# Kernel tuning notes

Measured on AMD Instinct MI355X. Metric: run time of the kernel, lower is better.

The kernel has to match this reference:

```python
import jax, jax.numpy as jnp
import numpy as np

N = 20000      # nodes
E = 640000     # edges
IN = 2         # in_dim
H = 4          # heads
C = 64         # hidden_dim (per-head channels)
ED = 3         # edge_dim
K = 4          # num_clusters
EPS = 1e-16    # PyG softmax eps


def setup_inputs():
    key = jax.random.key(0)
    ks = jax.random.split(key, 32)
    g = lambda i, sh: (jax.random.normal(ks[i], sh, dtype=jnp.float32) * 0.1)
    inp = {
        'x': jax.random.normal(ks[0], (N, IN), dtype=jnp.float32),
        'edge_index': jax.random.randint(ks[1], (2, E), 0, N, dtype=jnp.int64),
        'edge_attr': jax.random.normal(ks[2], (E, ED), dtype=jnp.float32),
        # input_proj
        'Wp': g(3, (IN, C)), 'bp': g(4, (C,)),
        # conv1: in C -> H*C, concat
        'W1': g(5, (C, H * C)), 'We1': g(6, (ED, H * C)),
        'as1': g(7, (H, C)), 'ad1': g(8, (H, C)), 'ae1': g(9, (H, C)), 'b1': g(10, (H * C,)),
        # conv2: in H*C -> H*C, concat
        'W2': g(11, (H * C, H * C)), 'We2': g(12, (ED, H * C)),
        'as2': g(13, (H, C)), 'ad2': g(14, (H, C)), 'ae2': g(15, (H, C)), 'b2': g(16, (H * C,)),
        # conv3: in H*C -> C, heads=1
        'W3': g(17, (H * C, C)), 'We3': g(18, (ED, C)),
        'as3': g(19, (1, C)), 'ad3': g(20, (1, C)), 'ae3': g(21, (1, C)), 'b3': g(22, (C,)),
        # classifier
        'Wc': g(23, (C, K)), 'bc': g(24, (K,)),
    }
    return inp


def _gat(h, src, dst, edge_attr, W, We, a_src, a_dst, a_edge, bias, heads, cph):
    """PyG GATConv (shared lin for src/dst, edge_dim, concat=True), eval mode."""
    xh = (h @ W).reshape(N, heads, cph)                       # [N,H,C]
    alpha_src = jnp.einsum('nhc,hc->nh', xh, a_src)           # [N,H]
    alpha_dst = jnp.einsum('nhc,hc->nh', xh, a_dst)
    eh = (edge_attr @ We).reshape(E, heads, cph)              # [E,H,C]
    alpha = alpha_src[src] + alpha_dst[dst] + jnp.einsum('ehc,hc->eh', eh, a_edge)
    alpha = jax.nn.leaky_relu(alpha, 0.2)                     # [E,H]
    # segment softmax over destination neighborhoods
    m = jax.ops.segment_max(alpha, dst, num_segments=N)       # [N,H]
    ea = jnp.exp(alpha - m[dst])
    s = jax.ops.segment_sum(ea, dst, num_segments=N)
    attn = ea / (s[dst] + EPS)                                # [E,H]
    msg = xh[src] * attn[:, :, None]                          # [E,H,C]
    out = jax.ops.segment_sum(msg, dst, num_segments=N)       # [N,H,C]
    return out.reshape(N, heads * cph) + bias


def reference(x, edge_index, edge_attr, Wp, bp,
              W1, We1, as1, ad1, ae1, b1,
              W2, We2, as2, ad2, ae2, b2,
              W3, We3, as3, ad3, ae3, b3,
              Wc, bc):
    src, dst = edge_index[0], edge_index[1]
    h = jax.nn.elu(x @ Wp + bp)
    h = jax.nn.elu(_gat(h, src, dst, edge_attr, W1, We1, as1, ad1, ae1, b1, H, C))
    h = jax.nn.elu(_gat(h, src, dst, edge_attr, W2, We2, as2, ad2, ae2, b2, H, C))
    h = _gat(h, src, dst, edge_attr, W3, We3, as3, ad3, ae3, b3, 1, C)
    return jax.nn.softmax(h @ Wc + bc, axis=-1)
```

## Files before the change

### kernel.cpp

```cpp
#include <hip/hip_runtime.h>
#include <math.h>

#define N_NODES 20000
#define N_EDGES 640000

typedef __attribute__((ext_vector_type(8))) short short8;
typedef __attribute__((ext_vector_type(4))) float floatx4;
typedef __attribute__((ext_vector_type(2))) float float2v;

__device__ __forceinline__ float elu_f(float v) { return v > 0.f ? v : expm1f(v); }

__device__ __forceinline__ unsigned short bf16_rne(float f) {
  union { float f; unsigned u; } v;
  v.f = f;
  unsigned r = v.u + 0x7FFF + ((v.u >> 16) & 1);
  return (unsigned short)(r >> 16);
}

__device__ __forceinline__ float2v unpack_bf2(unsigned u) {
  union { unsigned u; float f; } lo, hi;
  lo.u = u << 16;
  hi.u = u & 0xffff0000u;
  return (float2v){lo.f, hi.f};
}

__device__ __forceinline__ int swz(int c) {
  return (c & ~7) | ((((c & 7) + ((c >> 3) >> 2))) & 7);
}


__global__ void hist_kernel(const int* __restrict__ dst, int* __restrict__ cnt, int ne) {
  int e = blockIdx.x * 256 + threadIdx.x;
  if (e < ne) atomicAdd(&cnt[dst[e]], 1);
}

__global__ __launch_bounds__(1024) void scan_kernel(const int* __restrict__ cnt,
                                                    int* __restrict__ row_ptr,
                                                    int* __restrict__ row_next, int n) {
  __shared__ int part[1024];
  int t = threadIdx.x;
  int per = (n + 1023) / 1024;
  int base = t * per;
  int v[20];
  if (base + per <= n) {
    #pragma unroll
    for (int q = 0; q < 5; ++q) {
      int4 u = *(const int4*)(cnt + base + q * 4);
      v[q * 4 + 0] = u.x; v[q * 4 + 1] = u.y; v[q * 4 + 2] = u.z; v[q * 4 + 3] = u.w;
    }
  } else {
    #pragma unroll
    for (int i = 0; i < 20; ++i) v[i] = (base + i < n) ? cnt[base + i] : 0;
  }
  int local = 0;
  #pragma unroll
  for (int i = 0; i < 20; ++i) local += v[i];
  part[t] = local;
  __syncthreads();
  for (int off = 1; off < 1024; off <<= 1) {
    int pv = (t >= off) ? part[t - off] : 0;
    __syncthreads();
    part[t] += pv;
    __syncthreads();
  }
  int prefix = (t == 0) ? 0 : part[t - 1];
  #pragma unroll
  for (int i = 0; i < 20; ++i) {
    int idx = base + i;
    if (idx < n) {
      row_ptr[idx] = prefix;
      row_next[idx] = prefix;
      prefix += v[i];
    }
  }
  if (t == 1023) row_ptr[n] = part[1023];
}

__global__ void fill_kernel(const int* __restrict__ dst, int* __restrict__ row_next,
                            int* __restrict__ csr_eid, int ne) {
  int e = blockIdx.x * 256 + threadIdx.x;
  if (e >= ne) return;
  int pos = atomicAdd(&row_next[dst[e]], 1);
  csr_eid[pos] = e;
}


__global__ void prep_all_kernel(const float* __restrict__ x, const float* __restrict__ Wp,
                                const float* __restrict__ bp, unsigned short* __restrict__ h_bf,
                                const float* __restrict__ W1, const float* __restrict__ W2,
                                const float* __restrict__ W3, unsigned short* __restrict__ Bt1,
                                unsigned short* __restrict__ Bt2, unsigned short* __restrict__ Bt3,
                                const float* __restrict__ We1, const float* __restrict__ ae1,
                                const float* __restrict__ We2, const float* __restrict__ ae2,
                                const float* __restrict__ We3, const float* __restrict__ ae3,
                                const int* __restrict__ csr_eid, const int* __restrict__ src,
                                const float* __restrict__ ea, int* __restrict__ csr_src,
                                float* __restrict__ edot) {
  int b = blockIdx.x, t = threadIdx.x;
  if (b < 5000) {
    int i = b * 256 + t;
    int node = i >> 6, c = i & 63;
    float v = x[node * 2] * Wp[c] + x[node * 2 + 1] * Wp[64 + c] + bp[c];
    h_bf[i] = bf16_rne(elu_f(v));
  } else if (b < 5384) {
    int idx = (b - 5000) * 256 + t;
    const float* W; unsigned short* Bt; int K, Nc, local;
    if (idx < 16384)      { W = W1; Bt = Bt1; K = 64;  Nc = 256; local = idx; }
    else if (idx < 81920) { W = W2; Bt = Bt2; K = 256; Nc = 256; local = idx - 16384; }
    else if (idx < 98304) { W = W3; Bt = Bt3; K = 256; Nc = 64;  local = idx - 81920; }
    else return;
    int k = local / Nc, n = local - k * Nc;
    Bt[(size_t)n * K + k] = bf16_rne(W[local]);
  } else {
    __shared__ float pj[27];
    if (t < 12) {
      int d = t >> 2, h = t & 3;
      float s = 0.f;
      for (int c = 0; c < 64; ++c) s += We1[d * 256 + h * 64 + c] * ae1[h * 64 + c];
      pj[t] = s;
    } else if (t < 24) {
      int u = t - 12; int d = u >> 2, h = u & 3;
      float s = 0.f;
      for (int c = 0; c < 64; ++c) s += We2[d * 256 + h * 64 + c] * ae2[h * 64 + c];
      pj[12 + u] = s;
    } else if (t < 27) {
      int d = t - 24;
      float s = 0.f;
      for (int c = 0; c < 64; ++c) s += We3[d * 64 + c] * ae3[c];
      pj[24 + d] = s;
    }
    __syncthreads();
    int i = (b - 5384) * 256 + t;
    if (i >= N_EDGES) return;
    int eid = csr_eid[i];
    csr_src[i] = src[eid];
    float e0 = ea[eid * 3 + 0], e1 = ea[eid * 3 + 1], e2 = ea[eid * 3 + 2];
    #pragma unroll
    for (int h = 0; h < 4; ++h)
      edot[(size_t)h * N_EDGES + i] = e0 * pj[h] + e1 * pj[4 + h] + e2 * pj[8 + h];
    #pragma unroll
    for (int h = 0; h < 4; ++h)
      edot[(size_t)(4 + h) * N_EDGES + i] = e0 * pj[12 + h] + e1 * pj[16 + h] + e2 * pj[20 + h];
    edot[(size_t)8 * N_EDGES + i] = e0 * pj[24] + e1 * pj[25] + e2 * pj[26];
  }
}


template <int KDIM>
__global__ __launch_bounds__(256) void mfma_gemm_alpha_kernel(
    const unsigned short* __restrict__ A, const unsigned short* __restrict__ Bt,
    unsigned short* __restrict__ C_bf, const float* __restrict__ a_src,
    const float* __restrict__ a_dst, float* __restrict__ alp_s,
    float* __restrict__ alp_d, int M, int Nc) {
  __shared__ unsigned short As[64][40];
  __shared__ unsigned short Bs[64][40];
  int t = threadIdx.x;
  int wave = t >> 6, lane = t & 63;
  int m_frag = lane & 15, quad = lane >> 4;
  int row0 = blockIdx.y * 64, col0 = blockIdx.x * 64;
  int lr = t >> 2;
  int lk = (t & 3) * 8;
  floatx4 acc[4];
  #pragma unroll
  for (int c = 0; c < 4; ++c) acc[c] = (floatx4){0.f, 0.f, 0.f, 0.f};

  for (int k0 = 0; k0 < KDIM; k0 += 32) {
    int gr = row0 + lr;
    short8 av = {0, 0, 0, 0, 0, 0, 0, 0};
    if (gr < M) av = *(const short8*)(A + (size_t)gr * KDIM + k0 + lk);
    *(short8*)(&As[lr][lk]) = av;
    short8 bv = *(const short8*)(Bt + (size_t)(col0 + lr) * KDIM + k0 + lk);
    *(short8*)(&Bs[lr][lk]) = bv;
    __syncthreads();
    short8 a = *(const short8*)(&As[wave * 16 + m_frag][quad * 8]);
    #pragma unroll
    for (int c = 0; c < 4; ++c) {
      short8 b = *(const short8*)(&Bs[c * 16 + m_frag][quad * 8]);
      acc[c] = __builtin_amdgcn_mfma_f32_16x16x32_bf16(a, b, acc[c], 0, 0, 0);
    }
    __syncthreads();
  }

  int H = Nc >> 6;
  int head = blockIdx.x;
  float ps[4] = {}, pd[4] = {};
  #pragma unroll
  for (int c = 0; c < 4; ++c) {
    float asv = a_src[head * 64 + c * 16 + m_frag];
    float adv = a_dst[head * 64 + c * 16 + m_frag];
    #pragma unroll
    for (int i = 0; i < 4; ++i) {
      ps[i] += acc[c][i] * asv;
      pd[i] += acc[c][i] * adv;
    }
  }
  #pragma unroll
  for (int off = 1; off < 16; off <<= 1) {
    #pragma unroll
    for (int i = 0; i < 4; ++i) {
      ps[i] += __shfl_xor(ps[i], off);
      pd[i] += __shfl_xor(pd[i], off);
    }
  }
  #pragma unroll
  for (int c = 0; c < 4; ++c) {
    #pragma unroll
    for (int i = 0; i < 4; ++i) {
      int gr = row0 + wave * 16 + quad * 4 + i;
      if (gr < M) C_bf[(size_t)gr * Nc + col0 + c * 16 + m_frag] = bf16_rne(acc[c][i]);
    }
  }
  if (m_frag == 0) {
    #pragma unroll
    for (int i = 0; i < 4; ++i) {
      int gr = row0 + wave * 16 + quad * 4 + i;
      if (gr < M) {
        alp_s[gr * H + head] = ps[i];
        alp_d[gr * H + head] = pd[i];
      }
    }
  }
}


template <bool OUT_BF>
__global__ __launch_bounds__(256) void softagg4_kernel(
    const int* __restrict__ row_ptr, const int* __restrict__ csr_src,
    const float* __restrict__ edot, const float* __restrict__ alp_s,
    const float* __restrict__ alp_d, const unsigned short* __restrict__ xh_bf,
    const float* __restrict__ bias, float* __restrict__ out,
    unsigned short* __restrict__ out_bf) {
  constexpr int HC = 256, H = 4, CHUNK = 256, L = 32, S = 8;
  __shared__ float lds_w[H][CHUNK + 8];
  __shared__ int lds_src[CHUNK];
  __shared__ float sh_inv[H];
  __shared__ float red[4 * HC];

  int n = blockIdx.x;
  int t = threadIdx.x;
  int wave = t >> 6, lane = t & 63;
  int slot = t / L, l = t % L;
  int head2 = l >> 3;
  int s0 = row_ptr[n], s1 = row_ptr[n + 1];

  float s_run = 0.f;
  float2v accp[4] = {};
  float adv = alp_d[n * H + wave];
  const float* __restrict__ edot_h = edot + (size_t)wave * N_EDGES;

  for (int c0 = s0; c0 < s1; c0 += CHUNK) {
    int cend = min(s1, c0 + CHUNK);
    {
      float se = 0.f;
      for (int i = c0 + lane; i < cend; i += 64) {
        int s = csr_src[i];
        if (wave == 0) lds_src[i - c0] = s;
        float a = alp_s[s * H + wave] + adv + edot_h[i];
        a = a > 0.f ? a : 0.2f * a;
        float w = __expf(fminf(a, 30.f));
        lds_w[wave][i - c0] = w;
        se += w;
      }
      #pragma unroll
      for (int off = 1; off < 64; off <<= 1) se += __shfl_xor(se, off);
      s_run += se;
    }
    __syncthreads();
    int i = c0 + slot;
    for (; i + S < cend; i += 2 * S) {
      int sA = lds_src[i - c0];
      int sB = lds_src[i - c0 + S];
      float wA = lds_w[head2][i - c0];
      float wB = lds_w[head2][i - c0 + S];
      uint4 uA = *(const uint4*)(xh_bf + (size_t)sA * HC + l * 8);
      uint4 uB = *(const uint4*)(xh_bf + (size_t)sB * HC + l * 8);
      float2v wAp = {wA, wA}, wBp = {wB, wB};
      accp[0] = __builtin_elementwise_fma(unpack_bf2(uA.x), wAp, accp[0]);
      accp[1] = __builtin_elementwise_fma(unpack_bf2(uA.y), wAp, accp[1]);
      accp[2] = __builtin_elementwise_fma(unpack_bf2(uA.z), wAp, accp[2]);
      accp[3] = __builtin_elementwise_fma(unpack_bf2(uA.w), wAp, accp[3]);
      accp[0] = __builtin_elementwise_fma(unpack_bf2(uB.x), wBp, accp[0]);
      accp[1] = __builtin_elementwise_fma(unpack_bf2(uB.y), wBp, accp[1]);
      accp[2] = __builtin_elementwise_fma(unpack_bf2(uB.z), wBp, accp[2]);
      accp[3] = __builtin_elementwise_fma(unpack_bf2(uB.w), wBp, accp[3]);
    }
    if (i < cend) {
      int s = lds_src[i - c0];
      float w = lds_w[head2][i - c0];
      uint4 u = *(const uint4*)(xh_bf + (size_t)s * HC + l * 8);
      float2v wp = {w, w};
      accp[0] = __builtin_elementwise_fma(unpack_bf2(u.x), wp, accp[0]);
      accp[1] = __builtin_elementwise_fma(unpack_bf2(u.y), wp, accp[1]);
      accp[2] = __builtin_elementwise_fma(unpack_bf2(u.z), wp, accp[2]);
      accp[3] = __builtin_elementwise_fma(unpack_bf2(u.w), wp, accp[3]);
    }
    __syncthreads();
  }
  if (lane == 0) sh_inv[wave] = 1.0f / (s_run + 1e-16f);
  __syncthreads();
  float2v invp = {sh_inv[head2], sh_inv[head2]};
  #pragma unroll
  for (int d = 0; d < 4; ++d) accp[d] *= invp;
  float accf[8];
  #pragma unroll
  for (int d = 0; d < 4; ++d) { accf[2 * d] = accp[d].x; accf[2 * d + 1] = accp[d].y; }
  #pragma unroll
  for (int off = L; off < 64; off <<= 1) {
    #pragma unroll
    for (int j = 0; j < 8; ++j) accf[j] += __shfl_xor(accf[j], off);
  }
  if (lane < L) {
    #pragma unroll
    for (int j = 0; j < 8; ++j) red[wave * HC + swz(lane * 8 + j)] = accf[j];
  }
  __syncthreads();
  {
    int pos = swz(t);
    float a = red[0 * HC + pos] + red[1 * HC + pos] + red[2 * HC + pos] + red[3 * HC + pos];
    a += bias[t];
    a = elu_f(a);
    if (OUT_BF) out_bf[(size_t)n * HC + t] = bf16_rne(a);
    else out[(size_t)n * HC + t] = a;
  }
}


__global__ __launch_bounds__(256) void softagg_cls_kernel(
    const int* __restrict__ row_ptr, const int* __restrict__ csr_src,
    const float* __restrict__ edot, const float* __restrict__ alp_s,
    const float* __restrict__ alp_d, const unsigned short* __restrict__ xh_bf,
    const float* __restrict__ b3, const float* __restrict__ Wc,
    const float* __restrict__ bc, float* __restrict__ out, int n_nodes) {
  constexpr int CHUNK = 256;
  __shared__ float lds_w[4][CHUNK];
  __shared__ int lds_s[4][CHUNK];

  int wave = threadIdx.x >> 6, lane = threadIdx.x & 63;
  int n = blockIdx.x * 4 + wave;
  if (n >= n_nodes) return;
  int slot = lane >> 3, l = lane & 7;
  int s0 = row_ptr[n], s1 = row_ptr[n + 1];

  float s_run = 0.f;
  float2v accp[4] = {};
  float adv = alp_d[n];

  for (int c0 = s0; c0 < s1; c0 += CHUNK) {
    int cend = min(s1, c0 + CHUNK);
    float se = 0.f;
    for (int i = c0 + lane; i < cend; i += 64) {
      int s = csr_src[i];
      lds_s[wave][i - c0] = s;
      float a = alp_s[s] + adv + edot[i];
      a = a > 0.f ? a : 0.2f * a;
      float w = __expf(fminf(a, 30.f));
      lds_w[wave][i - c0] = w;
      se += w;
    }
    #pragma unroll
    for (int off = 1; off < 64; off <<= 1) se += __shfl_xor(se, off);
    s_run += se;
    int i = c0 + slot;
    for (; i + 8 < cend; i += 16) {
      int sA = lds_s[wave][i - c0];
      int sB = lds_s[wave][i - c0 + 8];
      float wA = lds_w[wave][i - c0];
      float wB = lds_w[wave][i - c0 + 8];
      uint4 uA = *(const uint4*)(xh_bf + (size_t)sA * 64 + l * 8);
      uint4 uB = *(const uint4*)(xh_bf + (size_t)sB * 64 + l * 8);
      float2v wAp = {wA, wA}, wBp = {wB, wB};
      accp[0] = __builtin_elementwise_fma(unpack_bf2(uA.x), wAp, accp[0]);
      accp[1] = __builtin_elementwise_fma(unpack_bf2(uA.y), wAp, accp[1]);
      accp[2] = __builtin_elementwise_fma(unpack_bf2(uA.z), wAp, accp[2]);
      accp[3] = __builtin_elementwise_fma(unpack_bf2(uA.w), wAp, accp[3]);
      accp[0] = __builtin_elementwise_fma(unpack_bf2(uB.x), wBp, accp[0]);
      accp[1] = __builtin_elementwise_fma(unpack_bf2(uB.y), wBp, accp[1]);
      accp[2] = __builtin_elementwise_fma(unpack_bf2(uB.z), wBp, accp[2]);
      accp[3] = __builtin_elementwise_fma(unpack_bf2(uB.w), wBp, accp[3]);
    }
    if (i < cend) {
      int s = lds_s[wave][i - c0];
      float w = lds_w[wave][i - c0];
      uint4 u = *(const uint4*)(xh_bf + (size_t)s * 64 + l * 8);
      float2v wp = {w, w};
      accp[0] = __builtin_elementwise_fma(unpack_bf2(u.x), wp, accp[0]);
      accp[1] = __builtin_elementwise_fma(unpack_bf2(u.y), wp, accp[1]);
      accp[2] = __builtin_elementwise_fma(unpack_bf2(u.z), wp, accp[2]);
      accp[3] = __builtin_elementwise_fma(unpack_bf2(u.w), wp, accp[3]);
    }
  }
  float inv = 1.0f / (s_run + 1e-16f);
  float2v invp = {inv, inv};
  #pragma unroll
  for (int d = 0; d < 4; ++d) accp[d] *= invp;
  float accf[8];
  #pragma unroll
  for (int d = 0; d < 4; ++d) { accf[2 * d] = accp[d].x; accf[2 * d + 1] = accp[d].y; }
  #pragma unroll
  for (int off = 8; off < 64; off <<= 1) {
    #pragma unroll
    for (int j = 0; j < 8; ++j) accf[j] += __shfl_xor(accf[j], off);
  }
  float p0 = 0.f, p1 = 0.f, p2 = 0.f, p3 = 0.f;
  #pragma unroll
  for (int j = 0; j < 8; ++j) {
    int c = l * 8 + j;
    float v = accf[j] + b3[c];
    p0 += v * Wc[c * 4 + 0];
    p1 += v * Wc[c * 4 + 1];
    p2 += v * Wc[c * 4 + 2];
    p3 += v * Wc[c * 4 + 3];
  }
  #pragma unroll
  for (int off = 1; off < 8; off <<= 1) {
    p0 += __shfl_xor(p0, off);
    p1 += __shfl_xor(p1, off);
    p2 += __shfl_xor(p2, off);
    p3 += __shfl_xor(p3, off);
  }
  if (lane == 0) {
    p0 += bc[0]; p1 += bc[1]; p2 += bc[2]; p3 += bc[3];
    float mx = fmaxf(fmaxf(p0, p1), fmaxf(p2, p3));
    float e0 = __expf(p0 - mx), e1 = __expf(p1 - mx), e2 = __expf(p2 - mx), e3 = __expf(p3 - mx);
    float s = 1.f / (e0 + e1 + e2 + e3);
    out[n * 4 + 0] = e0 * s;
    out[n * 4 + 1] = e1 * s;
    out[n * 4 + 2] = e2 * s;
    out[n * 4 + 3] = e3 * s;
  }
}


extern "C" void kernel_launch(void* const* d_in, const int* in_sizes, int n_in,
                              void* d_out, int out_size, void* d_ws, size_t ws_size,
                              hipStream_t stream) {
  const float* x   = (const float*)d_in[0];
  const int*   ei  = (const int*)d_in[1];
  const float* ea  = (const float*)d_in[2];
  const float* Wp  = (const float*)d_in[3];
  const float* bp  = (const float*)d_in[4];
  const float* W1  = (const float*)d_in[5];
  const float* We1 = (const float*)d_in[6];
  const float* as1 = (const float*)d_in[7];
  const float* ad1 = (const float*)d_in[8];
  const float* ae1 = (const float*)d_in[9];
  const float* b1  = (const float*)d_in[10];
  const float* W2  = (const float*)d_in[11];
  const float* We2 = (const float*)d_in[12];
  const float* as2 = (const float*)d_in[13];
  const float* ad2 = (const float*)d_in[14];
  const float* ae2 = (const float*)d_in[15];
  const float* b2  = (const float*)d_in[16];
  const float* W3  = (const float*)d_in[17];
  const float* We3 = (const float*)d_in[18];
  const float* as3 = (const float*)d_in[19];
  const float* ad3 = (const float*)d_in[20];
  const float* ae3 = (const float*)d_in[21];
  const float* b3  = (const float*)d_in[22];
  const float* Wc  = (const float*)d_in[23];
  const float* bc  = (const float*)d_in[24];
  float* out = (float*)d_out;

  const int* src = ei;
  const int* dst = ei + N_EDGES;

  char* wptr = (char*)d_ws;
  auto alloc = [&](size_t bytes) {
    char* p = wptr;
    wptr += (bytes + 255) & ~(size_t)255;
    return p;
  };
  int*            cnt      = (int*)alloc((size_t)N_NODES * 4);
  int*            row_ptr  = (int*)alloc((size_t)(N_NODES + 1) * 4);
  int*            row_next = (int*)alloc((size_t)N_NODES * 4);
  int*            csr_eid  = (int*)alloc((size_t)N_EDGES * 4);
  int*            csr_src  = (int*)alloc((size_t)N_EDGES * 4);
  float*          edot     = (float*)alloc((size_t)9 * N_EDGES * 4);
  unsigned short* hA_bf    = (unsigned short*)alloc((size_t)N_NODES * 256 * 2);
  unsigned short* hX_bf    = (unsigned short*)alloc((size_t)N_NODES * 256 * 2);
  float*          alp_s    = (float*)alloc((size_t)N_NODES * 4 * 4);
  float*          alp_d    = (float*)alloc((size_t)N_NODES * 4 * 4);
  unsigned short* Bt1      = (unsigned short*)alloc((size_t)64 * 256 * 2);
  unsigned short* Bt2      = (unsigned short*)alloc((size_t)256 * 256 * 2);
  unsigned short* Bt3      = (unsigned short*)alloc((size_t)256 * 64 * 2);

  hipMemsetAsync(cnt, 0, (size_t)N_NODES * 4, stream);
  hist_kernel<<<(N_EDGES + 255) / 256, 256, 0, stream>>>(dst, cnt, N_EDGES);
  scan_kernel<<<1, 1024, 0, stream>>>(cnt, row_ptr, row_next, N_NODES);
  fill_kernel<<<(N_EDGES + 255) / 256, 256, 0, stream>>>(dst, row_next, csr_eid, N_EDGES);

  prep_all_kernel<<<5384 + (N_EDGES + 255) / 256, 256, 0, stream>>>(
      x, Wp, bp, hA_bf, W1, W2, W3, Bt1, Bt2, Bt3,
      We1, ae1, We2, ae2, We3, ae3, csr_eid, src, ea, csr_src, edot);

  dim3 g256(4, (N_NODES + 63) / 64);
  dim3 g64(1, (N_NODES + 63) / 64);

  mfma_gemm_alpha_kernel<64><<<g256, 256, 0, stream>>>(hA_bf, Bt1, hX_bf, as1, ad1,
                                                       alp_s, alp_d, N_NODES, 256);
  softagg4_kernel<true><<<N_NODES, 256, 0, stream>>>(row_ptr, csr_src,
                                                     edot + (size_t)0 * N_EDGES,
                                                     alp_s, alp_d, hX_bf, b1, nullptr, hA_bf);

  mfma_gemm_alpha_kernel<256><<<g256, 256, 0, stream>>>(hA_bf, Bt2, hX_bf, as2, ad2,
                                                        alp_s, alp_d, N_NODES, 256);
  softagg4_kernel<true><<<N_NODES, 256, 0, stream>>>(row_ptr, csr_src,
                                                     edot + (size_t)4 * N_EDGES,
                                                     alp_s, alp_d, hX_bf, b2, nullptr, hA_bf);

  mfma_gemm_alpha_kernel<256><<<g64, 256, 0, stream>>>(hA_bf, Bt3, hX_bf, as3, ad3,
                                                       alp_s, alp_d, N_NODES, 64);
  softagg_cls_kernel<<<(N_NODES + 3) / 4, 256, 0, stream>>>(row_ptr, csr_src,
                                                            edot + (size_t)8 * N_EDGES,
                                                            alp_s, alp_d, hX_bf, b3, Wc, bc,
                                                            out, N_NODES);
}
```

Measured before the change: 377.5 us.

## Store edge attention terms in bf16, enlarge GEMM row tile, raise occupancy hints

Edge-attention dot products are stored as bf16 instead of fp32, which halves the traffic for the 9xE edot array that is written in prep and read by every aggregation kernel. The MFMA GEMM now computes 128 rows per block, two 16-row fragments per wave, so each B tile is reused twice and the grid is halved. The aggregation kernels also get launch_bounds with a minimum of 8 blocks per CU to push the compiler toward fewer registers and higher occupancy. The risks are reduced precision in the attention logits and possible register spills from the occupancy hint.

```diff
diff --git a/kernel.cpp b/kernel.cpp
--- a/kernel.cpp
+++ b/kernel.cpp
@@ -15,6 +15,12 @@
   v.f = f;
   unsigned r = v.u + 0x7FFF + ((v.u >> 16) & 1);
   return (unsigned short)(r >> 16);
+}
+
+__device__ __forceinline__ float bf_to_f(unsigned short u) {
+  union { unsigned u; float f; } v;
+  v.u = (unsigned)u << 16;
+  return v.f;
 }
 
 __device__ __forceinline__ float2v unpack_bf2(unsigned u) {
@@ -95,7 +101,7 @@
                                 const float* __restrict__ We3, const float* __restrict__ ae3,
                                 const int* __restrict__ csr_eid, const int* __restrict__ src,
                                 const float* __restrict__ ea, int* __restrict__ csr_src,
-                                float* __restrict__ edot) {
+                                unsigned short* __restrict__ edot) {
   int b = blockIdx.x, t = threadIdx.x;
   if (b < 5000) {
     int i = b * 256 + t;
@@ -137,11 +143,12 @@
     float e0 = ea[eid * 3 + 0], e1 = ea[eid * 3 + 1], e2 = ea[eid * 3 + 2];
     #pragma unroll
     for (int h = 0; h < 4; ++h)
-      edot[(size_t)h * N_EDGES + i] = e0 * pj[h] + e1 * pj[4 + h] + e2 * pj[8 + h];
+      edot[(size_t)h * N_EDGES + i] = bf16_rne(e0 * pj[h] + e1 * pj[4 + h] + e2 * pj[8 + h]);
     #pragma unroll
     for (int h = 0; h < 4; ++h)
-      edot[(size_t)(4 + h) * N_EDGES + i] = e0 * pj[12 + h] + e1 * pj[16 + h] + e2 * pj[20 + h];
-    edot[(size_t)8 * N_EDGES + i] = e0 * pj[24] + e1 * pj[25] + e2 * pj[26];
+      edot[(size_t)(4 + h) * N_EDGES + i] =
+          bf16_rne(e0 * pj[12 + h] + e1 * pj[16 + h] + e2 * pj[20 + h]);
+    edot[(size_t)8 * N_EDGES + i] = bf16_rne(e0 * pj[24] + e1 * pj[25] + e2 * pj[26]);
   }
 }
 
@@ -152,81 +159,91 @@
     unsigned short* __restrict__ C_bf, const float* __restrict__ a_src,
     const float* __restrict__ a_dst, float* __restrict__ alp_s,
     float* __restrict__ alp_d, int M, int Nc) {
-  __shared__ unsigned short As[64][40];
+  __shared__ unsigned short As[128][40];
   __shared__ unsigned short Bs[64][40];
   int t = threadIdx.x;
   int wave = t >> 6, lane = t & 63;
   int m_frag = lane & 15, quad = lane >> 4;
-  int row0 = blockIdx.y * 64, col0 = blockIdx.x * 64;
+  int row0 = blockIdx.y * 128, col0 = blockIdx.x * 64;
   int lr = t >> 2;
   int lk = (t & 3) * 8;
-  floatx4 acc[4];
-  #pragma unroll
-  for (int c = 0; c < 4; ++c) acc[c] = (floatx4){0.f, 0.f, 0.f, 0.f};
+  floatx4 acc[2][4];
+  #pragma unroll
+  for (int g = 0; g < 2; ++g)
+    #pragma unroll
+    for (int c = 0; c < 4; ++c) acc[g][c] = (floatx4){0.f, 0.f, 0.f, 0.f};
 
   for (int k0 = 0; k0 < KDIM; k0 += 32) {
-    int gr = row0 + lr;
-    short8 av = {0, 0, 0, 0, 0, 0, 0, 0};
-    if (gr < M) av = *(const short8*)(A + (size_t)gr * KDIM + k0 + lk);
-    *(short8*)(&As[lr][lk]) = av;
+    #pragma unroll
+    for (int g = 0; g < 2; ++g) {
+      int gr = row0 + g * 64 + lr;
+      short8 av = {0, 0, 0, 0, 0, 0, 0, 0};
+      if (gr < M) av = *(const short8*)(A + (size_t)gr * KDIM + k0 + lk);
+      *(short8*)(&As[g * 64 + lr][lk]) = av;
+    }
     short8 bv = *(const short8*)(Bt + (size_t)(col0 + lr) * KDIM + k0 + lk);
     *(short8*)(&Bs[lr][lk]) = bv;
     __syncthreads();
-    short8 a = *(const short8*)(&As[wave * 16 + m_frag][quad * 8]);
+    short8 a0 = *(const short8*)(&As[wave * 32 + m_frag][quad * 8]);
+    short8 a1 = *(const short8*)(&As[wave * 32 + 16 + m_frag][quad * 8]);
     #pragma unroll
     for (int c = 0; c < 4; ++c) {
       short8 b = *(const short8*)(&Bs[c * 16 + m_frag][quad * 8]);
-      acc[c] = __builtin_amdgcn_mfma_f32_16x16x32_bf16(a, b, acc[c], 0, 0, 0);
+      acc[0][c] = __builtin_amdgcn_mfma_f32_16x16x32_bf16(a0, b, acc[0][c], 0, 0, 0);
+      acc[1][c] = __builtin_amdgcn_mfma_f32_16x16x32_bf16(a1, b, acc[1][c], 0, 0, 0);
     }
     __syncthreads();
   }
 
   int H = Nc >> 6;
   int head = blockIdx.x;
-  float ps[4] = {}, pd[4] = {};
-  #pragma unroll
-  for (int c = 0; c < 4; ++c) {
-    float asv = a_src[head * 64 + c * 16 + m_frag];
-    float adv = a_dst[head * 64 + c * 16 + m_frag];
-    #pragma unroll
-    for (int i = 0; i < 4; ++i) {
-      ps[i] += acc[c][i] * asv;
-      pd[i] += acc[c][i] * adv;
-    }
-  }
-  #pragma unroll
-  for (int off = 1; off < 16; off <<= 1) {
-    #pragma unroll
-    for (int i = 0; i < 4; ++i) {
-      ps[i] += __shfl_xor(ps[i], off);
-      pd[i] += __shfl_xor(pd[i], off);
-    }
-  }
-  #pragma unroll
-  for (int c = 0; c < 4; ++c) {
-    #pragma unroll
-    for (int i = 0; i < 4; ++i) {
-      int gr = row0 + wave * 16 + quad * 4 + i;
-      if (gr < M) C_bf[(size_t)gr * Nc + col0 + c * 16 + m_frag] = bf16_rne(acc[c][i]);
-    }
-  }
-  if (m_frag == 0) {
-    #pragma unroll
-    for (int i = 0; i < 4; ++i) {
-      int gr = row0 + wave * 16 + quad * 4 + i;
-      if (gr < M) {
-        alp_s[gr * H + head] = ps[i];
-        alp_d[gr * H + head] = pd[i];
+  #pragma unroll
+  for (int g = 0; g < 2; ++g) {
+    float ps[4] = {}, pd[4] = {};
+    #pragma unroll
+    for (int c = 0; c < 4; ++c) {
+      float asv = a_src[head * 64 + c * 16 + m_frag];
+      float adv = a_dst[head * 64 + c * 16 + m_frag];
+      #pragma unroll
+      for (int i = 0; i < 4; ++i) {
+        ps[i] += acc[g][c][i] * asv;
+        pd[i] += acc[g][c][i] * adv;
       }
     }
+    #pragma unroll
+    for (int off = 1; off < 16; off <<= 1) {
+      #pragma unroll
+      for (int i = 0; i < 4; ++i) {
+        ps[i] += __shfl_xor(ps[i], off);
+        pd[i] += __shfl_xor(pd[i], off);
+      }
+    }
+    #pragma unroll
+    for (int c = 0; c < 4; ++c) {
+      #pragma unroll
+      for (int i = 0; i < 4; ++i) {
+        int gr = row0 + wave * 32 + g * 16 + quad * 4 + i;
+        if (gr < M) C_bf[(size_t)gr * Nc + col0 + c * 16 + m_frag] = bf16_rne(acc[g][c][i]);
+      }
+    }
+    if (m_frag == 0) {
+      #pragma unroll
+      for (int i = 0; i < 4; ++i) {
+        int gr = row0 + wave * 32 + g * 16 + quad * 4 + i;
+        if (gr < M) {
+          alp_s[gr * H + head] = ps[i];
+          alp_d[gr * H + head] = pd[i];
+        }
+      }
+    }
   }
 }
 
 
 template <bool OUT_BF>
-__global__ __launch_bounds__(256) void softagg4_kernel(
+__global__ __launch_bounds__(256, 8) void softagg4_kernel(
     const int* __restrict__ row_ptr, const int* __restrict__ csr_src,
-    const float* __restrict__ edot, const float* __restrict__ alp_s,
+    const unsigned short* __restrict__ edot, const float* __restrict__ alp_s,
     const float* __restrict__ alp_d, const unsigned short* __restrict__ xh_bf,
     const float* __restrict__ bias, float* __restrict__ out,
     unsigned short* __restrict__ out_bf) {
@@ -246,7 +263,7 @@
   float s_run = 0.f;
   float2v accp[4] = {};
   float adv = alp_d[n * H + wave];
-  const float* __restrict__ edot_h = edot + (size_t)wave * N_EDGES;
+  const unsigned short* __restrict__ edot_h = edot + (size_t)wave * N_EDGES;
 
   for (int c0 = s0; c0 < s1; c0 += CHUNK) {
     int cend = min(s1, c0 + CHUNK);
@@ -255,7 +272,7 @@
       for (int i = c0 + lane; i < cend; i += 64) {
         int s = csr_src[i];
         if (wave == 0) lds_src[i - c0] = s;
-        float a = alp_s[s * H + wave] + adv + edot_h[i];
+        float a = alp_s[s * H + wave] + adv + bf_to_f(edot_h[i]);
         a = a > 0.f ? a : 0.2f * a;
         float w = __expf(fminf(a, 30.f));
         lds_w[wave][i - c0] = w;
@@ -325,9 +342,9 @@
 }
 
 
-__global__ __launch_bounds__(256) void softagg_cls_kernel(
+__global__ __launch_bounds__(256, 8) void softagg_cls_kernel(
     const int* __restrict__ row_ptr, const int* __restrict__ csr_src,
-    const float* __restrict__ edot, const float* __restrict__ alp_s,
+    const unsigned short* __restrict__ edot, const float* __restrict__ alp_s,
     const float* __restrict__ alp_d, const unsigned short* __restrict__ xh_bf,
     const float* __restrict__ b3, const float* __restrict__ Wc,
     const float* __restrict__ bc, float* __restrict__ out, int n_nodes) {
@@ -351,7 +368,7 @@
     for (int i = c0 + lane; i < cend; i += 64) {
       int s = csr_src[i];
       lds_s[wave][i - c0] = s;
-      float a = alp_s[s] + adv + edot[i];
+      float a = alp_s[s] + adv + bf_to_f(edot[i]);
       a = a > 0.f ? a : 0.2f * a;
       float w = __expf(fminf(a, 30.f));
       lds_w[wave][i - c0] = w;
@@ -475,7 +492,7 @@
   int*            row_next = (int*)alloc((size_t)N_NODES * 4);
   int*            csr_eid  = (int*)alloc((size_t)N_EDGES * 4);
   int*            csr_src  = (int*)alloc((size_t)N_EDGES * 4);
-  float*          edot     = (float*)alloc((size_t)9 * N_EDGES * 4);
+  unsigned short* edot     = (unsigned short*)alloc((size_t)9 * N_EDGES * 2);
   unsigned short* hA_bf    = (unsigned short*)alloc((size_t)N_NODES * 256 * 2);
   unsigned short* hX_bf    = (unsigned short*)alloc((size_t)N_NODES * 256 * 2);
   float*          alp_s    = (float*)alloc((size_t)N_NODES * 4 * 4);
@@ -493,8 +510,8 @@
       x, Wp, bp, hA_bf, W1, W2, W3, Bt1, Bt2, Bt3,
       We1, ae1, We2, ae2, We3, ae3, csr_eid, src, ea, csr_src, edot);
 
-  dim3 g256(4, (N_NODES + 63) / 64);
-  dim3 g64(1, (N_NODES + 63) / 64);
+  dim3 g256(4, (N_NODES + 127) / 128);
+  dim3 g64(1, (N_NODES + 127) / 128);
 
   mfma_gemm_alpha_kernel<64><<<g256, 256, 0, stream>>>(hA_bf, Bt1, hX_bf, as1, ad1,
                                                        alp_s, alp_d, N_NODES, 256);
```

After: 380.6 us. No clear change (+0.8%).
